# Performance work log

Measured on AMD Instinct MI355X. Metric: run time of the kernel, lower is better.

The kernel has to match this reference:

```python
import jax, jax.numpy as jnp
import numpy as np

B, T, D = 4, 2048, 1024
EPS = 1e-5


def _layernorm(x, g, b):
    mu = jnp.mean(x, axis=-1, keepdims=True)
    var = jnp.var(x, axis=-1, keepdims=True)
    return (x - mu) * jax.lax.rsqrt(var + EPS) * g + b


def setup_inputs() -> dict:
    key = jax.random.key(0)
    ks = jax.random.split(key, 16)
    s = lambda fan_in: 1.0 / np.sqrt(fan_in)
    return {
        "x": jax.random.normal(ks[0], (B, T, D), dtype=jnp.float32),
        "ln1_g": jnp.ones((D,), jnp.float32),
        "ln1_b": jnp.zeros((D,), jnp.float32),
        "Wqkv": jax.random.uniform(ks[1], (D, 3 * D), jnp.float32, -s(D), s(D)),
        "bqkv": jnp.zeros((3 * D,), jnp.float32),
        "Wproj": jax.random.uniform(ks[2], (D, D), jnp.float32, -s(D), s(D)),
        "bproj": jnp.zeros((D,), jnp.float32),
        "ln2_g": jnp.ones((D,), jnp.float32),
        "ln2_b": jnp.zeros((D,), jnp.float32),
        "W1": jax.random.uniform(ks[3], (D, 4 * D), jnp.float32, -s(D), s(D)),
        "b1": jnp.zeros((4 * D,), jnp.float32),
        "W2": jax.random.uniform(ks[4], (4 * D, D), jnp.float32, -s(4 * D), s(4 * D)),
        "b2": jnp.zeros((D,), jnp.float32),
    }


def reference(x, ln1_g, ln1_b, Wqkv, bqkv, Wproj, bproj, ln2_g, ln2_b, W1, b1, W2, b2):
    # NOTE: no residual connections in the original Block.
    h = _layernorm(x, ln1_g, ln1_b)
    kqv = h @ Wqkv + bqkv                      # [B,T,3D]
    k, q, v = jnp.split(kqv, 3, axis=-1)       # split order: k, q, v
    # Original scales by 1/sqrt(k.size(-1)) AFTER transposing k -> 1/sqrt(T).
    scores = jnp.einsum("btd,bsd->bts", q, k) * (1.0 / np.sqrt(T))
    causal = jnp.tril(jnp.ones((T, T), dtype=bool))
    scores = jnp.where(causal, scores, -jnp.inf)
    attn = jax.nn.softmax(scores, axis=-1)
    a = jnp.einsum("bts,bsd->btd", attn, v)
    a = a @ Wproj + bproj
    h2 = _layernorm(a, ln2_g, ln2_b)
    m = jax.nn.gelu(h2 @ W1 + b1, approximate=True)
    return m @ W2 + b2
```

## Files before the change

kernel.cpp:

```cpp
#include <hip/hip_runtime.h>
#include <hip/hip_bf16.h>

typedef __hip_bfloat16 bf16;
typedef __bf16 bf16x8 __attribute__((ext_vector_type(8)));
typedef __bf16 bf16x4 __attribute__((ext_vector_type(4)));
typedef __bf16 bf16x2 __attribute__((ext_vector_type(2)));
typedef float f32x4 __attribute__((ext_vector_type(4)));

static constexpr int Bq = 4, Tq = 2048, Dq = 1024;

__device__ inline float b2f(bf16 h) { return __bfloat162float(h); }
__device__ inline bf16 f2b(float f) { return __float2bfloat16(f); }

__device__ __forceinline__ void gload_lds16(const bf16* g, bf16* lds_wave_base) {
    __builtin_amdgcn_global_load_lds((const __attribute__((address_space(1))) void*)g,
                                     (__attribute__((address_space(3))) void*)lds_wave_base,
                                     16, 0, 0);
}

__device__ __forceinline__ float fast_gelu(float x) {
    float u = x * (0.7978845608028654f + 0.03567740814183427f * x * x);
    float e = __builtin_amdgcn_exp2f(-2.885390081777927f * u);
    return x * __builtin_amdgcn_rcpf(1.f + e);
}

__device__ inline void ld4f(const float* p, float* v) {
    float4 t = *reinterpret_cast<const float4*>(p);
    v[0] = t.x; v[1] = t.y; v[2] = t.z; v[3] = t.w;
}
__device__ inline void ld4f(const bf16* p, float* v) {
    bf16x4 t = *reinterpret_cast<const bf16x4*>(p);
    v[0] = (float)t[0]; v[1] = (float)t[1]; v[2] = (float)t[2]; v[3] = (float)t[3];
}

template <typename Tin>
__global__ void ln_kernel(const Tin* __restrict__ x, const float* __restrict__ g,
                          const float* __restrict__ b, bf16* __restrict__ out)
{
    const int row = blockIdx.x;
    const int tid = threadIdx.x;
    const int s0 = tid * 4;
    const Tin* xr = x + (size_t)row * Dq;
    bf16* orow = out + (size_t)row * Dq;
    float v[4], gv[4], bv[4];
    ld4f(xr + s0, v);
    ld4f(g + s0, gv);
    ld4f(b + s0, bv);
    float sum = v[0] + v[1] + v[2] + v[3];
    float sq = v[0]*v[0] + v[1]*v[1] + v[2]*v[2] + v[3]*v[3];
    for (int o = 32; o > 0; o >>= 1) { sum += __shfl_xor(sum, o); sq += __shfl_xor(sq, o); }
    __shared__ float ssum[4], ssq[4];
    const int w = tid >> 6;
    if ((tid & 63) == 0) { ssum[w] = sum; ssq[w] = sq; }
    __syncthreads();
    const float ts = ssum[0] + ssum[1] + ssum[2] + ssum[3];
    const float tq = ssq[0] + ssq[1] + ssq[2] + ssq[3];
    const float mean = ts / Dq;
    const float rs = rsqrtf(tq / Dq - mean * mean + 1e-5f);
    bf16x4 o4;
    #pragma unroll
    for (int i = 0; i < 4; ++i) o4[i] = (__bf16)((v[i] - mean) * rs * gv[i] + bv[i]);
    *reinterpret_cast<bf16x4*>(orow + s0) = o4;
}

__global__ void transpose_f2b_kernel(const float* __restrict__ in, bf16* __restrict__ out,
                                     long ldin, long ldout)
{
    __shared__ float tile[64][65];
    const int c0 = blockIdx.x * 64, r0 = blockIdx.y * 64;
    const int tid = threadIdx.x;
    const int tx = tid & 63, ty = tid >> 6;
    #pragma unroll
    for (int i = 0; i < 16; ++i) {
        int r = ty + i * 4;
        tile[r][tx] = in[(size_t)(r0 + r) * ldin + c0 + tx];
    }
    __syncthreads();
    const int px = tid & 31, cy = tid >> 5;
    #pragma unroll
    for (int i = 0; i < 8; ++i) {
        int cc = cy + i * 8;
        bf16x2 p;
        p[0] = (__bf16)tile[px * 2][cc];
        p[1] = (__bf16)tile[px * 2 + 1][cc];
        *reinterpret_cast<bf16x2*>(&out[(size_t)(c0 + cc) * ldout + r0 + px * 2]) = p;
    }
}

__global__ void transpose_b2b_kernel(const bf16* __restrict__ in, bf16* __restrict__ out,
                                     long ldin, long ldout, long inBatch, long outBatch)
{
    __shared__ bf16 tile[64][66];
    const bf16* ip = in + (size_t)blockIdx.z * inBatch;
    bf16* op = out + (size_t)blockIdx.z * outBatch;
    const int c0 = blockIdx.x * 64, r0 = blockIdx.y * 64;
    const int tid = threadIdx.x;
    const int tx = tid & 31, ty = tid >> 5;
    #pragma unroll
    for (int i = 0; i < 8; ++i) {
        int r = ty + i * 8;
        *reinterpret_cast<bf16x2*>(&tile[r][tx * 2]) =
            *reinterpret_cast<const bf16x2*>(&ip[(size_t)(r0 + r) * ldin + c0 + tx * 2]);
    }
    __syncthreads();
    #pragma unroll
    for (int i = 0; i < 8; ++i) {
        int cc = ty + i * 8;
        bf16x2 p;
        p[0] = tile[tx * 2][cc];
        p[1] = tile[tx * 2 + 1][cc];
        *reinterpret_cast<bf16x2*>(&op[(size_t)(c0 + cc) * ldout + r0 + tx * 2]) = p;
    }
}

__global__ void rowsum_kernel(const bf16* __restrict__ attn, float* __restrict__ invl)
{
    const int row = blockIdx.x;
    const int t = row & (Tq - 1);
    const bf16* base = attn + (size_t)(row >> 11) * Tq * Tq + (size_t)t * Tq;
    const int tid = threadIdx.x;
    const int len = t + 1;
    const int s0 = tid * 8;
    bf16x8 v = *reinterpret_cast<const bf16x8*>(base + s0);
    float sum = 0.f;
    #pragma unroll
    for (int i = 0; i < 8; ++i) sum += (s0 + i < len) ? (float)v[i] : 0.f;
    for (int o = 32; o > 0; o >>= 1) sum += __shfl_xor(sum, o);
    __shared__ float sred[4];
    const int w = tid >> 6;
    if ((tid & 63) == 0) sred[w] = sum;
    __syncthreads();
    if (tid == 0) invl[row] = 1.f / (sred[0] + sred[1] + sred[2] + sred[3]);
}

__global__ void gemm128(const bf16* __restrict__ A, const bf16* __restrict__ Bt,
                        const float* __restrict__ bias, const float* __restrict__ rowscale,
                        bf16* __restrict__ Cb, float* __restrict__ Cf,
                        int K, long lda, long ldb, long ldc,
                        long sA, long sB, long sC,
                        float scale, int act, int tri, int causalK)
{
    int bx, by;
    if (tri) {
        const int lin = blockIdx.x;
        int t = (int)((sqrtf(8.f * lin + 1.f) - 1.f) * 0.5f);
        while ((t + 1) * (t + 2) / 2 <= lin) ++t;
        while (t * (t + 1) / 2 > lin) --t;
        by = t; bx = lin - t * (t + 1) / 2;
    } else {
        const int gx = gridDim.x, gy = gridDim.y;
        const int lin = blockIdx.x + gx * blockIdx.y;
        const int band = lin & 7;
        const int idx = lin >> 3;
        bx = idx % gx;
        by = band * (gy >> 3) + idx / gx;
    }

    const int m0 = by * 128, n0 = bx * 128;
    const int Kend = causalK ? min(K, m0 + 128) : K;

    __shared__ bf16 As[128 * 32];
    __shared__ bf16 Bs[128 * 32];

    const bf16* Ab = A + (size_t)blockIdx.z * sA;
    const bf16* Bb = Bt + (size_t)blockIdx.z * sB;
    const int tid = threadIdx.x;
    const int wid = tid >> 6, lane = tid & 63;
    const int wr = wid >> 1, wc = wid & 1;
    const int l15 = lane & 15, quad = lane >> 4;

    const int srow = wid * 16 + (lane >> 2);
    const int scol = (((lane & 3) ^ ((srow >> 1) & 3))) * 8;
    const bf16* agp0 = Ab + (size_t)(m0 + srow) * lda + scol;
    const bf16* agp1 = Ab + (size_t)(m0 + 64 + srow) * lda + scol;
    const bf16* bgp0 = Bb + (size_t)(n0 + srow) * ldb + scol;
    const bf16* bgp1 = Bb + (size_t)(n0 + 64 + srow) * ldb + scol;
    bf16* aw0 = As + wid * 512;
    bf16* aw1 = As + 2048 + wid * 512;
    bf16* bw0 = Bs + wid * 512;
    bf16* bw1 = Bs + 2048 + wid * 512;

    const int xsw = (l15 >> 1) & 3;
    const int afo = (wr * 64 + l15) * 32 + (quad ^ xsw) * 8;
    const int bfo = (wc * 64 + l15) * 32 + (quad ^ xsw) * 8;

    f32x4 acc[4][4];
    #pragma unroll
    for (int i = 0; i < 4; ++i)
        #pragma unroll
        for (int j = 0; j < 4; ++j) acc[i][j] = (f32x4){0.f, 0.f, 0.f, 0.f};

    for (int k0 = 0; k0 < Kend; k0 += 32) {
        gload_lds16(agp0 + k0, aw0);
        gload_lds16(agp1 + k0, aw1);
        gload_lds16(bgp0 + k0, bw0);
        gload_lds16(bgp1 + k0, bw1);
        __syncthreads();

        bf16x8 af[4], bff[4];
        #pragma unroll
        for (int i = 0; i < 4; ++i) af[i] = *reinterpret_cast<const bf16x8*>(As + afo + i * 512);
        #pragma unroll
        for (int j = 0; j < 4; ++j) bff[j] = *reinterpret_cast<const bf16x8*>(Bs + bfo + j * 512);
        #pragma unroll
        for (int i = 0; i < 4; ++i)
            #pragma unroll
            for (int j = 0; j < 4; ++j)
                acc[i][j] = __builtin_amdgcn_mfma_f32_16x16x32_bf16(af[i], bff[j], acc[i][j], 0, 0, 0);

        __syncthreads();
    }

    const float* rsb = rowscale ? rowscale + (size_t)blockIdx.z * Tq : nullptr;

    #pragma unroll
    for (int i = 0; i < 4; ++i) {
        const int row = m0 + wr * 64 + i * 16 + quad * 4;
        #pragma unroll
        for (int j = 0; j < 4; ++j) {
            const int col = n0 + wc * 64 + j * 16 + l15;
            const float bv = bias ? bias[col] : 0.f;
            #pragma unroll
            for (int r = 0; r < 4; ++r) {
                float vv = scale * acc[i][j][r] + bv;
                if (act == 1) vv = fast_gelu(vv);
                else if (act == 2)
                    vv = (col <= row + r) ? __builtin_amdgcn_exp2f(1.4426950408889634f * vv) : 0.f;
                if (rsb) vv *= rsb[row + r];
                const size_t idx2 = (size_t)(row + r) * ldc + col + (size_t)blockIdx.z * sC;
                if (Cf) Cf[idx2] = vv;
                else    Cb[idx2] = f2b(vv);
            }
        }
    }
}

extern "C" void kernel_launch(void* const* d_in, const int* in_sizes, int n_in,
                              void* d_out, int out_size, void* d_ws, size_t ws_size,
                              hipStream_t stream)
{
    (void)in_sizes; (void)n_in; (void)out_size; (void)ws_size;
    const float* x     = (const float*)d_in[0];
    const float* ln1g  = (const float*)d_in[1];
    const float* ln1b  = (const float*)d_in[2];
    const float* Wqkv  = (const float*)d_in[3];
    const float* bqkv  = (const float*)d_in[4];
    const float* Wproj = (const float*)d_in[5];
    const float* bproj = (const float*)d_in[6];
    const float* ln2g  = (const float*)d_in[7];
    const float* ln2b  = (const float*)d_in[8];
    const float* W1    = (const float*)d_in[9];
    const float* b1    = (const float*)d_in[10];
    const float* W2    = (const float*)d_in[11];
    const float* b2    = (const float*)d_in[12];
    float* out = (float*)d_out;

    char* ws = (char*)d_ws;
    size_t off = 0;
    auto alloc = [&](size_t elems) { bf16* p = (bf16*)(ws + off); off += elems * sizeof(bf16); return p; };
    bf16* WqkvT  = alloc(3072UL * 1024);
    bf16* WprojT = alloc(1024UL * 1024);
    bf16* W1T    = alloc(4096UL * 1024);
    bf16* W2T    = alloc(1024UL * 4096);
    bf16* h      = alloc(8192UL * 1024);
    bf16* kqv    = alloc(8192UL * 3072);
    bf16* vT     = alloc(4UL * 1024 * 2048);
    bf16* attn   = alloc(4UL * 2048 * 2048);
    float* invl  = (float*)alloc(8192UL * 2);
    bf16* a   = h;
    bf16* p   = kqv;
    bf16* h2  = kqv + 8192UL * 1024;
    bf16* m   = kqv + 2UL * 8192 * 1024;

    const long T3D = (long)Tq * 3072, TT = (long)Tq * Tq, DT = (long)Dq * Tq, TD = (long)Tq * Dq;

    transpose_f2b_kernel<<<dim3(48, 16), 256, 0, stream>>>(Wqkv,  WqkvT,  3072L, 1024L);
    transpose_f2b_kernel<<<dim3(16, 16), 256, 0, stream>>>(Wproj, WprojT, 1024L, 1024L);
    transpose_f2b_kernel<<<dim3(64, 16), 256, 0, stream>>>(W1,   W1T,    4096L, 1024L);
    transpose_f2b_kernel<<<dim3(16, 64), 256, 0, stream>>>(W2,   W2T,    1024L, 4096L);

    ln_kernel<float><<<8192, 256, 0, stream>>>(x, ln1g, ln1b, h);

    gemm128<<<dim3(24, 64, 1), 256, 0, stream>>>(h, WqkvT, bqkv, nullptr, kqv, nullptr,
        1024, 1024L, 1024L, 3072L, 0L, 0L, 0L, 1.f, 0, 0, 0);

    transpose_b2b_kernel<<<dim3(16, 32, 4), 256, 0, stream>>>(kqv + 2048, vT, 3072L, 2048L, T3D, DT);

    gemm128<<<dim3(136, 1, 4), 256, 0, stream>>>(kqv + 1024, kqv, nullptr, nullptr, attn, nullptr,
        1024, 3072L, 3072L, 2048L, T3D, T3D, TT, 0.022097086912079608f, 2, 1, 0);

    rowsum_kernel<<<8192, 256, 0, stream>>>(attn, invl);

    gemm128<<<dim3(8, 16, 4), 256, 0, stream>>>(attn, vT, nullptr, invl, a, nullptr,
        2048, 2048L, 2048L, 1024L, TT, DT, TD, 1.f, 0, 0, 1);

    gemm128<<<dim3(8, 64, 1), 256, 0, stream>>>(a, WprojT, bproj, nullptr, p, nullptr,
        1024, 1024L, 1024L, 1024L, 0L, 0L, 0L, 1.f, 0, 0, 0);

    ln_kernel<bf16><<<8192, 256, 0, stream>>>(p, ln2g, ln2b, h2);

    gemm128<<<dim3(32, 64, 1), 256, 0, stream>>>(h2, W1T, b1, nullptr, m, nullptr,
        1024, 1024L, 1024L, 4096L, 0L, 0L, 0L, 1.f, 1, 0, 0);

    gemm128<<<dim3(8, 64, 1), 256, 0, stream>>>(m, W2T, b2, nullptr, nullptr, out,
        4096, 4096L, 4096L, 1024L, 0L, 0L, 0L, 1.f, 0, 0, 0);
}
```

Baseline: 552.7 us.

## Fuse softmax row-sum into attention GEMM and merge prep kernels

Removes the separate row-sum pass over the attention matrix by accumulating row sums with an extra MFMA against a ones vector inside the attn·V GEMM, and normalizing in the epilogue. Merges the four weight transposes and first LayerNorm into a single prep kernel, and templates the GEMM on its mode flags so branches are compile-time. This trades one full read of the attention matrix and several launches for additional MFMA work in the attn·V GEMM.

After: 524.1 us. 1.05x faster.

```diff
diff --git a/kernel.cpp b/kernel.cpp
--- a/kernel.cpp
+++ b/kernel.cpp
@@ -34,10 +34,10 @@
 }
 
 template <typename Tin>
-__global__ void ln_kernel(const Tin* __restrict__ x, const float* __restrict__ g,
-                          const float* __restrict__ b, bf16* __restrict__ out)
-{
-    const int row = blockIdx.x;
+__device__ __forceinline__ void ln_body(const Tin* __restrict__ x, const float* __restrict__ g,
+                                        const float* __restrict__ b, bf16* __restrict__ out,
+                                        int row, float* sred)
+{
     const int tid = threadIdx.x;
     const int s0 = tid * 4;
     const Tin* xr = x + (size_t)row * Dq;
@@ -49,12 +49,11 @@
     float sum = v[0] + v[1] + v[2] + v[3];
     float sq = v[0]*v[0] + v[1]*v[1] + v[2]*v[2] + v[3]*v[3];
     for (int o = 32; o > 0; o >>= 1) { sum += __shfl_xor(sum, o); sq += __shfl_xor(sq, o); }
-    __shared__ float ssum[4], ssq[4];
     const int w = tid >> 6;
-    if ((tid & 63) == 0) { ssum[w] = sum; ssq[w] = sq; }
+    if ((tid & 63) == 0) { sred[w] = sum; sred[4 + w] = sq; }
     __syncthreads();
-    const float ts = ssum[0] + ssum[1] + ssum[2] + ssum[3];
-    const float tq = ssq[0] + ssq[1] + ssq[2] + ssq[3];
+    const float ts = sred[0] + sred[1] + sred[2] + sred[3];
+    const float tq = sred[4] + sred[5] + sred[6] + sred[7];
     const float mean = ts / Dq;
     const float rs = rsqrtf(tq / Dq - mean * mean + 1e-5f);
     bf16x4 o4;
@@ -63,17 +62,37 @@
     *reinterpret_cast<bf16x4*>(orow + s0) = o4;
 }
 
-__global__ void transpose_f2b_kernel(const float* __restrict__ in, bf16* __restrict__ out,
-                                     long ldin, long ldout)
-{
-    __shared__ float tile[64][65];
-    const int c0 = blockIdx.x * 64, r0 = blockIdx.y * 64;
+__global__ void ln_kernel(const bf16* __restrict__ x, const float* __restrict__ g,
+                          const float* __restrict__ b, bf16* __restrict__ out)
+{
+    __shared__ float sred[8];
+    ln_body(x, g, b, out, blockIdx.x, sred);
+}
+
+__global__ void prep_kernel(const float* __restrict__ x, const float* __restrict__ g,
+                            const float* __restrict__ b, bf16* __restrict__ h,
+                            const float* __restrict__ Wqkv, bf16* __restrict__ WqkvT,
+                            const float* __restrict__ Wproj, bf16* __restrict__ WprojT,
+                            const float* __restrict__ W1, bf16* __restrict__ W1T,
+                            const float* __restrict__ W2, bf16* __restrict__ W2T)
+{
+    __shared__ float smem[64 * 65];
+    int id = blockIdx.x;
+    if (id < 8192) { ln_body(x, g, b, h, id, smem); return; }
+    id -= 8192;
+    const float* src; bf16* dst; long ldin, ldout; int gx;
+    if (id < 768)       { src = Wqkv;  dst = WqkvT;  ldin = 3072; ldout = 1024; gx = 48; }
+    else if (id < 1024) { id -= 768;  src = Wproj; dst = WprojT; ldin = 1024; ldout = 1024; gx = 16; }
+    else if (id < 2048) { id -= 1024; src = W1;    dst = W1T;    ldin = 4096; ldout = 1024; gx = 64; }
+    else                { id -= 2048; src = W2;    dst = W2T;    ldin = 1024; ldout = 4096; gx = 16; }
+    const int c0 = (id % gx) * 64, r0 = (id / gx) * 64;
     const int tid = threadIdx.x;
     const int tx = tid & 63, ty = tid >> 6;
+    float (*tile)[65] = reinterpret_cast<float(*)[65]>(smem);
     #pragma unroll
     for (int i = 0; i < 16; ++i) {
         int r = ty + i * 4;
-        tile[r][tx] = in[(size_t)(r0 + r) * ldin + c0 + tx];
+        tile[r][tx] = src[(size_t)(r0 + r) * ldin + c0 + tx];
     }
     __syncthreads();
     const int px = tid & 31, cy = tid >> 5;
@@ -83,7 +102,7 @@
         bf16x2 p;
         p[0] = (__bf16)tile[px * 2][cc];
         p[1] = (__bf16)tile[px * 2 + 1][cc];
-        *reinterpret_cast<bf16x2*>(&out[(size_t)(c0 + cc) * ldout + r0 + px * 2]) = p;
+        *reinterpret_cast<bf16x2*>(&dst[(size_t)(c0 + cc) * ldout + r0 + px * 2]) = p;
     }
 }
 
@@ -113,35 +132,15 @@
     }
 }
 
-__global__ void rowsum_kernel(const bf16* __restrict__ attn, float* __restrict__ invl)
-{
-    const int row = blockIdx.x;
-    const int t = row & (Tq - 1);
-    const bf16* base = attn + (size_t)(row >> 11) * Tq * Tq + (size_t)t * Tq;
-    const int tid = threadIdx.x;
-    const int len = t + 1;
-    const int s0 = tid * 8;
-    bf16x8 v = *reinterpret_cast<const bf16x8*>(base + s0);
-    float sum = 0.f;
-    #pragma unroll
-    for (int i = 0; i < 8; ++i) sum += (s0 + i < len) ? (float)v[i] : 0.f;
-    for (int o = 32; o > 0; o >>= 1) sum += __shfl_xor(sum, o);
-    __shared__ float sred[4];
-    const int w = tid >> 6;
-    if ((tid & 63) == 0) sred[w] = sum;
-    __syncthreads();
-    if (tid == 0) invl[row] = 1.f / (sred[0] + sred[1] + sred[2] + sred[3]);
-}
-
+template <int ACT, int TRI, int CK, int FR>
 __global__ void gemm128(const bf16* __restrict__ A, const bf16* __restrict__ Bt,
-                        const float* __restrict__ bias, const float* __restrict__ rowscale,
+                        const float* __restrict__ bias,
                         bf16* __restrict__ Cb, float* __restrict__ Cf,
                         int K, long lda, long ldb, long ldc,
-                        long sA, long sB, long sC,
-                        float scale, int act, int tri, int causalK)
+                        long sA, long sB, long sC, float scale)
 {
     int bx, by;
-    if (tri) {
+    if (TRI) {
         const int lin = blockIdx.x;
         int t = (int)((sqrtf(8.f * lin + 1.f) - 1.f) * 0.5f);
         while ((t + 1) * (t + 2) / 2 <= lin) ++t;
@@ -157,7 +156,7 @@
     }
 
     const int m0 = by * 128, n0 = bx * 128;
-    const int Kend = causalK ? min(K, m0 + 128) : K;
+    const int Kend = CK ? min(K, m0 + 128) : K;
 
     __shared__ bf16 As[128 * 32];
     __shared__ bf16 Bs[128 * 32];
@@ -190,6 +189,15 @@
         #pragma unroll
         for (int j = 0; j < 4; ++j) acc[i][j] = (f32x4){0.f, 0.f, 0.f, 0.f};
 
+    f32x4 acc_l[4];
+    bf16x8 ones;
+    if (FR) {
+        #pragma unroll
+        for (int i = 0; i < 4; ++i) acc_l[i] = (f32x4){0.f, 0.f, 0.f, 0.f};
+        #pragma unroll
+        for (int i = 0; i < 8; ++i) ones[i] = (__bf16)1.0f;
+    }
+
     for (int k0 = 0; k0 < Kend; k0 += 32) {
         gload_lds16(agp0 + k0, aw0);
         gload_lds16(agp1 + k0, aw1);
@@ -207,11 +215,14 @@
             #pragma unroll
             for (int j = 0; j < 4; ++j)
                 acc[i][j] = __builtin_amdgcn_mfma_f32_16x16x32_bf16(af[i], bff[j], acc[i][j], 0, 0, 0);
+        if (FR) {
+            #pragma unroll
+            for (int i = 0; i < 4; ++i)
+                acc_l[i] = __builtin_amdgcn_mfma_f32_16x16x32_bf16(af[i], ones, acc_l[i], 0, 0, 0);
+        }
 
         __syncthreads();
     }
-
-    const float* rsb = rowscale ? rowscale + (size_t)blockIdx.z * Tq : nullptr;
 
     #pragma unroll
     for (int i = 0; i < 4; ++i) {
@@ -223,10 +234,10 @@
             #pragma unroll
             for (int r = 0; r < 4; ++r) {
                 float vv = scale * acc[i][j][r] + bv;
-                if (act == 1) vv = fast_gelu(vv);
-                else if (act == 2)
+                if (ACT == 1) vv = fast_gelu(vv);
+                else if (ACT == 2)
                     vv = (col <= row + r) ? __builtin_amdgcn_exp2f(1.4426950408889634f * vv) : 0.f;
-                if (rsb) vv *= rsb[row + r];
+                if (FR) vv *= __builtin_amdgcn_rcpf(acc_l[i][r]);
                 const size_t idx2 = (size_t)(row + r) * ldc + col + (size_t)blockIdx.z * sC;
                 if (Cf) Cf[idx2] = vv;
                 else    Cb[idx2] = f2b(vv);
@@ -266,7 +277,6 @@
     bf16* kqv    = alloc(8192UL * 3072);
     bf16* vT     = alloc(4UL * 1024 * 2048);
     bf16* attn   = alloc(4UL * 2048 * 2048);
-    float* invl  = (float*)alloc(8192UL * 2);
     bf16* a   = h;
     bf16* p   = kqv;
     bf16* h2  = kqv + 8192UL * 1024;
@@ -274,34 +284,28 @@
 
     const long T3D = (long)Tq * 3072, TT = (long)Tq * Tq, DT = (long)Dq * Tq, TD = (long)Tq * Dq;
 
-    transpose_f2b_kernel<<<dim3(48, 16), 256, 0, stream>>>(Wqkv,  WqkvT,  3072L, 1024L);
-    transpose_f2b_kernel<<<dim3(16, 16), 256, 0, stream>>>(Wproj, WprojT, 1024L, 1024L);
-    transpose_f2b_kernel<<<dim3(64, 16), 256, 0, stream>>>(W1,   W1T,    4096L, 1024L);
-    transpose_f2b_kernel<<<dim3(16, 64), 256, 0, stream>>>(W2,   W2T,    1024L, 4096L);
-
-    ln_kernel<float><<<8192, 256, 0, stream>>>(x, ln1g, ln1b, h);
-
-    gemm128<<<dim3(24, 64, 1), 256, 0, stream>>>(h, WqkvT, bqkv, nullptr, kqv, nullptr,
-        1024, 1024L, 1024L, 3072L, 0L, 0L, 0L, 1.f, 0, 0, 0);
+    prep_kernel<<<11264, 256, 0, stream>>>(x, ln1g, ln1b, h,
+                                           Wqkv, WqkvT, Wproj, WprojT, W1, W1T, W2, W2T);
+
+    gemm128<0,0,0,0><<<dim3(24, 64, 1), 256, 0, stream>>>(h, WqkvT, bqkv, kqv, nullptr,
+        1024, 1024L, 1024L, 3072L, 0L, 0L, 0L, 1.f);
 
     transpose_b2b_kernel<<<dim3(16, 32, 4), 256, 0, stream>>>(kqv + 2048, vT, 3072L, 2048L, T3D, DT);
 
-    gemm128<<<dim3(136, 1, 4), 256, 0, stream>>>(kqv + 1024, kqv, nullptr, nullptr, attn, nullptr,
-        1024, 3072L, 3072L, 2048L, T3D, T3D, TT, 0.022097086912079608f, 2, 1, 0);
-
-    rowsum_kernel<<<8192, 256, 0, stream>>>(attn, invl);
-
-    gemm128<<<dim3(8, 16, 4), 256, 0, stream>>>(attn, vT, nullptr, invl, a, nullptr,
-        2048, 2048L, 2048L, 1024L, TT, DT, TD, 1.f, 0, 0, 1);
-
-    gemm128<<<dim3(8, 64, 1), 256, 0, stream>>>(a, WprojT, bproj, nullptr, p, nullptr,
-        1024, 1024L, 1024L, 1024L, 0L, 0L, 0L, 1.f, 0, 0, 0);
-
-    ln_kernel<bf16><<<8192, 256, 0, stream>>>(p, ln2g, ln2b, h2);
-
-    gemm128<<<dim3(32, 64, 1), 256, 0, stream>>>(h2, W1T, b1, nullptr, m, nullptr,
-        1024, 1024L, 1024L, 4096L, 0L, 0L, 0L, 1.f, 1, 0, 0);
-
-    gemm128<<<dim3(8, 64, 1), 256, 0, stream>>>(m, W2T, b2, nullptr, nullptr, out,
-        4096, 4096L, 4096L, 1024L, 0L, 0L, 0L, 1.f, 0, 0, 0);
-}
+    gemm128<2,1,0,0><<<dim3(136, 1, 4), 256, 0, stream>>>(kqv + 1024, kqv, nullptr, attn, nullptr,
+        1024, 3072L, 3072L, 2048L, T3D, T3D, TT, 0.022097086912079608f);
+
+    gemm128<0,0,1,1><<<dim3(8, 16, 4), 256, 0, stream>>>(attn, vT, nullptr, a, nullptr,
+        2048, 2048L, 2048L, 1024L, TT, DT, TD, 1.f);
+
+    gemm128<0,0,0,0><<<dim3(8, 64, 1), 256, 0, stream>>>(a, WprojT, bproj, p, nullptr,
+        1024, 1024L, 1024L, 1024L, 0L, 0L, 0L, 1.f);
+
+    ln_kernel<<<8192, 256, 0, stream>>>(p, ln2g, ln2b, h2);
+
+    gemm128<1,0,0,0><<<dim3(32, 64, 1), 256, 0, stream>>>(h2, W1T, b1, m, nullptr,
+        1024, 1024L, 1024L, 4096L, 0L, 0L, 0L, 1.f);
+
+    gemm128<0,0,0,0><<<dim3(8, 64, 1), 256, 0, stream>>>(m, W2T, b2, nullptr, out,
+        4096, 4096L, 4096L, 1024L, 0L, 0L, 0L, 1.f);
+}
```
